# Kernel tuning notes

Hardware: AMD Instinct MI355X
Metric: run time of the kernel (lower is better)

The kernel has to match this reference:

```python
import jax, jax.numpy as jnp
import numpy as np

B, N, D_IN, D_MEM, LAYERS = 8, 2048, 128, 128, 3


def setup_inputs() -> dict:
    key = jax.random.key(0)
    k1, k2, k3, k4 = jax.random.split(key, 4)
    inputs = jax.random.normal(k1, (B, N, D_IN), dtype=jnp.float32)
    # attention-derived adjacency: nonnegative weights
    out_adj = jax.random.uniform(k2, (B, N, N), dtype=jnp.float32)
    # per-layer Linear weights (all layers 128->128 here, stacked) with
    # torch nn.Linear-style init scale 1/sqrt(fan_in)
    scale = 1.0 / np.sqrt(D_IN)
    W = jax.random.uniform(k3, (LAYERS, D_IN, D_MEM), minval=-scale, maxval=scale, dtype=jnp.float32)
    b = jax.random.uniform(k4, (LAYERS, D_MEM), minval=-scale, maxval=scale, dtype=jnp.float32)
    return {"inputs": inputs, "out_adj": out_adj, "W": W, "b": b}


def reference(inputs, out_adj, W, b):
    # GCN.forward (eval mode; dropout = identity)
    adj = out_adj  # [B, N, N]
    denom = jnp.sum(adj, axis=2, keepdims=True) + 1.0  # [B, N, 1]
    outputs = inputs  # [B, N, D]
    for l in range(W.shape[0]):
        Ax = jnp.einsum('bij,bjd->bid', adj, outputs)      # aggregate
        AxW = Ax @ W[l] + b[l]                             # per-layer linear
        outputs = jax.nn.relu(AxW / denom)                 # normalize + activate
    return outputs
```

## Files before the change

### kernel.cpp

```cpp
#include <hip/hip_runtime.h>

#define NN 2048
#define DD 128

typedef _Float16 f16x8 __attribute__((ext_vector_type(8)));
typedef float f32x4 __attribute__((ext_vector_type(4)));


__global__ __launch_bounds__(256) void prep_kernel(
    const float* __restrict__ W, _Float16* __restrict__ Wt) {
  int idx = blockIdx.x * 256 + threadIdx.x;
  int l = idx >> 14, r = idx & 16383, d = r >> 7, k = r & 127;
  Wt[idx] = (_Float16)W[l * 16384 + k * 128 + d];
}

__global__ __launch_bounds__(256) void prepAdj_kernel(
    const float* __restrict__ adj, _Float16* __restrict__ adjH,
    float* __restrict__ rdg) {
  __shared__ float rs[16][4];
  const int bx = blockIdx.x, tid = threadIdx.x;
  const int it = bx & 127, batch = bx >> 7;
  const int lane = tid & 63, wave = tid >> 6;
  const int quad = lane >> 4, l15 = lane & 15;

  const float* Ap = adj + ((size_t)(batch * NN) + it * 16 + l15) * NN + quad * 8;
  _Float16* Hp = adjH + (size_t)batch * NN * NN + ((size_t)it * 64) * 512 + lane * 8;

  float s = 0.f;
#pragma unroll
  for (int j = 0; j < 16; ++j) {
    const int ct = wave + 4 * j;
    float4 a0 = *(const float4*)(Ap + ct * 32);
    float4 a1 = *(const float4*)(Ap + ct * 32 + 4);
    s += ((a0.x + a0.y) + (a0.z + a0.w)) + ((a1.x + a1.y) + (a1.z + a1.w));
    f16x8 h = {(_Float16)a0.x, (_Float16)a0.y, (_Float16)a0.z, (_Float16)a0.w,
               (_Float16)a1.x, (_Float16)a1.y, (_Float16)a1.z, (_Float16)a1.w};
    *(f16x8*)(Hp + (size_t)ct * 512) = h;
  }
  s += __shfl_xor(s, 16);
  s += __shfl_xor(s, 32);
  if (lane < 16) rs[lane][wave] = s;
  __syncthreads();
  if (tid < 16) {
    float t = rs[tid][0] + rs[tid][1] + rs[tid][2] + rs[tid][3];
    rdg[batch * NN + it * 16 + tid] = 1.0f / (t + 1.0f);
  }
}

__global__ __launch_bounds__(256) void transposeX_kernel(
    const float* __restrict__ X, _Float16* __restrict__ Xt) {
  const int bx = blockIdx.x, tid = threadIdx.x;
  const int batch = bx & 7, nt = bx >> 3;
  const int lane = tid & 63, wave = tid >> 6;
  const int quad = lane >> 4, l15 = lane & 15;
  const size_t batA = (size_t)batch * (128 * NN);
#pragma unroll
  for (int dtl = 0; dtl < 2; ++dtl) {
    const int dt = wave * 2 + dtl;
    const float* Xp = X + ((size_t)(batch * NN) + nt * 32 + quad * 8) * DD + dt * 16 + l15;
    f16x8 v;
#pragma unroll
    for (int e = 0; e < 8; ++e) v[e] = (_Float16)Xp[(size_t)e * DD];
    *(f16x8*)(Xt + batA + ((size_t)(dt * 64 + nt)) * 512 + lane * 8) = v;
  }
}

__device__ __forceinline__ void epiGemm(const float (*Xs)[132],
    const _Float16* __restrict__ Wf, int d0, int quad, int l15,
    f32x4 (&o)[2][2]) {
#pragma unroll
  for (int kk = 0; kk < 128; kk += 32) {
    f16x8 a0 = *(const f16x8*)(Wf + (d0 + l15) * DD + kk + quad * 8);
    f16x8 a1 = *(const f16x8*)(Wf + (d0 + 16 + l15) * DD + kk + quad * 8);
#pragma unroll
    for (int fi = 0; fi < 2; ++fi) {
      const float* xp = &Xs[fi * 16 + l15][kk + quad * 8];
      f16x8 b = {(_Float16)xp[0], (_Float16)xp[1], (_Float16)xp[2], (_Float16)xp[3],
                 (_Float16)xp[4], (_Float16)xp[5], (_Float16)xp[6], (_Float16)xp[7]};
      o[0][fi] = __builtin_amdgcn_mfma_f32_16x16x32_f16(a0, b, o[0][fi], 0, 0, 0);
      o[1][fi] = __builtin_amdgcn_mfma_f32_16x16x32_f16(a1, b, o[1][fi], 0, 0, 0);
    }
  }
}

template<int MODE>
__global__ __launch_bounds__(256, 4) void aggT_kernel(
    const _Float16* __restrict__ adjH, const float* __restrict__ rdg,
    const _Float16* __restrict__ At, const float* __restrict__ bias,
    const _Float16* __restrict__ WA, const _Float16* __restrict__ WB,
    _Float16* __restrict__ Yout, float* __restrict__ out) {
  __shared__ float Xs[32][132];
  __shared__ float bsh[128];
  __shared__ float rdsh[32];

  const int tid = threadIdx.x, bx = blockIdx.x;
  const int batch = bx & 7, i0 = (bx >> 3) * 32;
  const int lane = tid & 63, wave = tid >> 6;
  const int quad = lane >> 4, l15 = lane & 15, d0 = wave * 32;

  const size_t batA = (size_t)batch * (128 * NN);
  const size_t batB = (size_t)batch * ((size_t)NN * NN);
  const int it0 = i0 >> 4;
  const _Float16* Ap0 = At + batA + ((size_t)(2 * wave) * 64) * 512 + lane * 8;
  const _Float16* Ap1 = At + batA + ((size_t)(2 * wave + 1) * 64) * 512 + lane * 8;
  const _Float16* Bp0 = adjH + batB + ((size_t)it0 * 64) * 512 + lane * 8;
  const _Float16* Bp1 = adjH + batB + ((size_t)(it0 + 1) * 64) * 512 + lane * 8;

  if (tid < 128) bsh[tid] = bias[tid];
  if (tid < 32) rdsh[tid] = rdg[batch * NN + i0 + tid];
  __syncthreads();

  f32x4 acc[2][2] = {};
  f16x8 qa0[2], qa1[2], qb0[2], qb1[2];
#define LDT(ct, s)                                  \
  { qa0[s] = *(const f16x8*)(Ap0 + (ct) * 512);     \
    qa1[s] = *(const f16x8*)(Ap1 + (ct) * 512);     \
    qb0[s] = *(const f16x8*)(Bp0 + (ct) * 512);     \
    qb1[s] = *(const f16x8*)(Bp1 + (ct) * 512); }
#define MMT(s)                                                                          \
  { acc[0][0] = __builtin_amdgcn_mfma_f32_16x16x32_f16(qa0[s], qb0[s], acc[0][0], 0, 0, 0); \
    acc[0][1] = __builtin_amdgcn_mfma_f32_16x16x32_f16(qa0[s], qb1[s], acc[0][1], 0, 0, 0); \
    acc[1][0] = __builtin_amdgcn_mfma_f32_16x16x32_f16(qa1[s], qb0[s], acc[1][0], 0, 0, 0); \
    acc[1][1] = __builtin_amdgcn_mfma_f32_16x16x32_f16(qa1[s], qb1[s], acc[1][1], 0, 0, 0); }

  LDT(0, 0)
  LDT(1, 1)
#pragma unroll
  for (int ct = 0; ct < 64; ct += 2) {
    MMT(0)
    if (ct + 2 < 64) LDT(ct + 2, 0)
    MMT(1)
    if (ct + 3 < 64) LDT(ct + 3, 1)
  }
#undef LDT
#undef MMT

  const float rv0 = rdsh[l15], rv1 = rdsh[16 + l15];

  f32x4 accY[2][2];

  if (MODE == 0) {
#pragma unroll
    for (int df = 0; df < 2; ++df)
#pragma unroll
      for (int fi = 0; fi < 2; ++fi)
#pragma unroll
        for (int r = 0; r < 4; ++r)
          Xs[fi * 16 + l15][d0 + df * 16 + quad * 4 + r] = acc[df][fi][r];
    __syncthreads();
    f32x4 acc2[2][2] = {};
    epiGemm(Xs, WA, d0, quad, l15, acc2);
    __syncthreads();
#pragma unroll
    for (int df = 0; df < 2; ++df)
#pragma unroll
      for (int fi = 0; fi < 2; ++fi)
#pragma unroll
        for (int r = 0; r < 4; ++r) {
          int d = d0 + df * 16 + quad * 4 + r;
          float rv = fi ? rv1 : rv0;
          Xs[fi * 16 + l15][d] = fmaxf((acc2[df][fi][r] + bsh[d]) * rv, 0.f);
        }
    __syncthreads();
    f32x4 acc3[2][2] = {};
    epiGemm(Xs, WB, d0, quad, l15, acc3);
#pragma unroll
    for (int df = 0; df < 2; ++df)
#pragma unroll
      for (int fi = 0; fi < 2; ++fi) accY[df][fi] = acc3[df][fi];
  } else {
#pragma unroll
    for (int df = 0; df < 2; ++df)
#pragma unroll
      for (int fi = 0; fi < 2; ++fi)
#pragma unroll
        for (int r = 0; r < 4; ++r) {
          int d = d0 + df * 16 + quad * 4 + r;
          float rv = fi ? rv1 : rv0;
          Xs[fi * 16 + l15][d] = fmaxf((acc[df][fi][r] + bsh[d]) * rv, 0.f);
        }
    __syncthreads();
    if (MODE == 2) {
      float* outB = out + (size_t)(batch * NN + i0) * DD;
#pragma unroll
      for (int u = 0; u < 4; ++u) {
        int c = tid + 256 * u;
        int i = c >> 5, f4 = (c & 31) * 4;
        *(float4*)(outB + (size_t)i * DD + f4) = *(const float4*)&Xs[i][f4];
      }
      return;
    }
    f32x4 acc2[2][2] = {};
    epiGemm(Xs, WA, d0, quad, l15, acc2);
#pragma unroll
    for (int df = 0; df < 2; ++df)
#pragma unroll
      for (int fi = 0; fi < 2; ++fi) accY[df][fi] = acc2[df][fi];
  }

  __syncthreads();
  _Float16* Yst = (_Float16*)Xs;
#pragma unroll
  for (int df = 0; df < 2; ++df)
#pragma unroll
    for (int fi = 0; fi < 2; ++fi)
#pragma unroll
      for (int r = 0; r < 4; ++r)
        Yst[(d0 + df * 16 + quad * 4 + r) * 40 + fi * 16 + l15] =
            (_Float16)accY[df][fi][r];
  __syncthreads();
  const int nt = i0 >> 5;
  _Float16* Yb = Yout + batA;
#pragma unroll
  for (int dtl = 0; dtl < 2; ++dtl) {
    const int dt = 2 * wave + dtl;
    f16x8 v = *(const f16x8*)(&Yst[(dt * 16 + l15) * 40 + quad * 8]);
    *(f16x8*)(Yb + ((size_t)(dt * 64 + nt)) * 512 + lane * 8) = v;
  }
}

__global__ __launch_bounds__(256) void gemmY_kernel(
    const float* __restrict__ X, const _Float16* __restrict__ Wt,
    _Float16* __restrict__ Yt) {
  const int bx = blockIdx.x;
  const int batch = bx & 7, n0 = (bx >> 3) * 32;
  const int tid = threadIdx.x, lane = tid & 63, wave = tid >> 6;
  const int quad = lane >> 4, l15 = lane & 15, d0 = wave * 32;
  const float* Xb = X + (size_t)(batch * NN + n0) * DD;
  f32x4 acc[2][2] = {};
#pragma unroll
  for (int kk = 0; kk < 128; kk += 32) {
    f16x8 a0 = *(const f16x8*)(Wt + (d0 + l15) * DD + kk + quad * 8);
    f16x8 a1 = *(const f16x8*)(Wt + (d0 + 16 + l15) * DD + kk + quad * 8);
#pragma unroll
    for (int fi = 0; fi < 2; ++fi) {
      const float* xp = Xb + (size_t)(fi * 16 + l15) * DD + kk + quad * 8;
      float4 x0 = *(const float4*)xp;
      float4 x1 = *(const float4*)(xp + 4);
      f16x8 b = {(_Float16)x0.x, (_Float16)x0.y, (_Float16)x0.z, (_Float16)x0.w,
                 (_Float16)x1.x, (_Float16)x1.y, (_Float16)x1.z, (_Float16)x1.w};
      acc[0][fi] = __builtin_amdgcn_mfma_f32_16x16x32_f16(a0, b, acc[0][fi], 0, 0, 0);
      acc[1][fi] = __builtin_amdgcn_mfma_f32_16x16x32_f16(a1, b, acc[1][fi], 0, 0, 0);
    }
  }
  _Float16* YtB = Yt + (size_t)batch * DD * NN;
#pragma unroll
  for (int df = 0; df < 2; ++df)
#pragma unroll
    for (int fi = 0; fi < 2; ++fi)
#pragma unroll
      for (int r = 0; r < 4; ++r)
        YtB[(size_t)(d0 + df * 16 + quad * 4 + r) * NN + n0 + fi * 16 + l15] =
            (_Float16)acc[df][fi][r];
}

template<bool LAST>
__global__ __launch_bounds__(256) void agg_kernel(
    const float* __restrict__ adj, const _Float16* __restrict__ Yt,
    const float* __restrict__ bias, const _Float16* __restrict__ Wn,
    _Float16* __restrict__ Ytn, float* __restrict__ out) {
  __shared__ _Float16 Bs[2][32 * 64];
  __shared__ float Xs[32][132];
  __shared__ float bsh[128];
  __shared__ float rd[32];

  const int tid = threadIdx.x, bx = blockIdx.x;
  const int batch = bx & 7, i0 = (bx >> 3) * 32;
  const int lane = tid & 63, wave = tid >> 6;
  const int quad = lane >> 4, l15 = lane & 15, d0 = wave * 32;
  const int ai = tid >> 3, ac = tid & 7;
  const int sc = ac ^ (ai & 7);

  const float* adjR = adj + (size_t)(batch * NN + i0 + ai) * NN + ac * 8;
  const _Float16* YtB = Yt + (size_t)batch * DD * NN;
  const _Float16* Ya0 = YtB + (size_t)(d0 + l15) * NN;
  const _Float16* Ya1 = YtB + (size_t)(d0 + 16 + l15) * NN;

  if (tid < 128) bsh[tid] = bias[tid];

  f32x4 acc[2][2] = {};
  float rowsum = 0.f;

  float4 av0 = *(const float4*)(adjR);
  float4 av1 = *(const float4*)(adjR + 4);
  f16x8 a[2][2];
#pragma unroll
  for (int k2 = 0; k2 < 2; ++k2) {
    a[k2][0] = *(const f16x8*)(Ya0 + k2 * 32 + quad * 8);
    a[k2][1] = *(const f16x8*)(Ya1 + k2 * 32 + quad * 8);
  }

  for (int ko = 0; ko < 32; ++ko) {
    rowsum += ((av0.x + av0.y) + (av0.z + av0.w)) + ((av1.x + av1.y) + (av1.z + av1.w));
    f16x8 h = {(_Float16)av0.x, (_Float16)av0.y, (_Float16)av0.z, (_Float16)av0.w,
               (_Float16)av1.x, (_Float16)av1.y, (_Float16)av1.z, (_Float16)av1.w};
    *(f16x8*)(&Bs[ko & 1][ai * 64 + sc * 8]) = h;
    f16x8 an[2][2];
    if (ko < 31) {
      const int kb = (ko + 1) * 64;
      av0 = *(const float4*)(adjR + kb);
      av1 = *(const float4*)(adjR + kb + 4);
#pragma unroll
      for (int k2 = 0; k2 < 2; ++k2) {
        an[k2][0] = *(const f16x8*)(Ya0 + kb + k2 * 32 + quad * 8);
        an[k2][1] = *(const f16x8*)(Ya1 + kb + k2 * 32 + quad * 8);
      }
    }
    __syncthreads();
    const _Float16* B = Bs[ko & 1];
#pragma unroll
    for (int k2 = 0; k2 < 2; ++k2)
#pragma unroll
      for (int fi = 0; fi < 2; ++fi) {
        const int row = fi * 16 + l15;
        const int ch = (k2 * 4 + quad) ^ (row & 7);
        f16x8 b = *(const f16x8*)(&B[row * 64 + ch * 8]);
        acc[0][fi] = __builtin_amdgcn_mfma_f32_16x16x32_f16(a[k2][0], b, acc[0][fi], 0, 0, 0);
        acc[1][fi] = __builtin_amdgcn_mfma_f32_16x16x32_f16(a[k2][1], b, acc[1][fi], 0, 0, 0);
      }
#pragma unroll
    for (int k2 = 0; k2 < 2; ++k2) { a[k2][0] = an[k2][0]; a[k2][1] = an[k2][1]; }
  }

  rowsum += __shfl_xor(rowsum, 1);
  rowsum += __shfl_xor(rowsum, 2);
  rowsum += __shfl_xor(rowsum, 4);
  if (ac == 0) rd[ai] = 1.0f / (rowsum + 1.0f);
  __syncthreads();

#pragma unroll
  for (int df = 0; df < 2; ++df)
#pragma unroll
    for (int fi = 0; fi < 2; ++fi)
#pragma unroll
      for (int r = 0; r < 4; ++r) {
        int d = d0 + df * 16 + quad * 4 + r;
        int i = fi * 16 + l15;
        Xs[i][d] = fmaxf((acc[df][fi][r] + bsh[d]) * rd[i], 0.f);
      }
  __syncthreads();

  if (LAST) {
    float* outB = out + (size_t)(batch * NN + i0) * DD;
#pragma unroll
    for (int u = 0; u < 4; ++u) {
      int c = tid + 256 * u;
      int i = c >> 5, f4 = (c & 31) * 4;
      *(float4*)(outB + (size_t)i * DD + f4) = *(const float4*)&Xs[i][f4];
    }
  } else {
    f32x4 acc2[2][2] = {};
    epiGemm(Xs, Wn, d0, quad, l15, acc2);
    _Float16* YnB = Ytn + (size_t)batch * DD * NN;
#pragma unroll
    for (int df = 0; df < 2; ++df)
#pragma unroll
      for (int fi = 0; fi < 2; ++fi)
#pragma unroll
        for (int r = 0; r < 4; ++r)
          YnB[(size_t)(d0 + df * 16 + quad * 4 + r) * NN + i0 + fi * 16 + l15] =
              (_Float16)acc2[df][fi][r];
  }
}

extern "C" void kernel_launch(void* const* d_in, const int* in_sizes, int n_in,
                              void* d_out, int out_size, void* d_ws, size_t ws_size,
                              hipStream_t stream) {
  const float* x0   = (const float*)d_in[0];
  const float* adj  = (const float*)d_in[1];
  const float* W    = (const float*)d_in[2];
  const float* bias = (const float*)d_in[3];
  float* out = (float*)d_out;

  _Float16* Wt   = (_Float16*)d_ws;
  float*    rdg  = (float*)((char*)d_ws + (1u << 17));
  _Float16* Xt   = (_Float16*)((char*)d_ws + (1u << 20));
  _Float16* Y1t  = (_Float16*)((char*)d_ws + (5u << 20));
  _Float16* Y2t  = (_Float16*)((char*)d_ws + (9u << 20));
  _Float16* adjH = (_Float16*)((char*)d_ws + (16u << 20));

  const bool big = ws_size >= (80ull << 20);

  dim3 blk(256);
  prep_kernel<<<192, blk, 0, stream>>>(W, Wt);
  if (big) {
    prepAdj_kernel  <<<1024, blk, 0, stream>>>(adj, adjH, rdg);
    transposeX_kernel<<<512, blk, 0, stream>>>(x0, Xt);
    aggT_kernel<0><<<512, blk, 0, stream>>>(adjH, rdg, Xt, bias, Wt, Wt + 16384, Y1t, nullptr);
    aggT_kernel<1><<<512, blk, 0, stream>>>(adjH, rdg, Y1t, bias + 128, Wt + 32768, nullptr, Y2t, nullptr);
    aggT_kernel<2><<<512, blk, 0, stream>>>(adjH, rdg, Y2t, bias + 256, nullptr, nullptr, nullptr, out);
  } else {
    _Float16* YtA  = Xt;
    _Float16* YtB_ = (_Float16*)d_out;
    gemmY_kernel<<<512, blk, 0, stream>>>(x0, Wt, YtA);
    agg_kernel<false><<<512, blk, 0, stream>>>(adj, YtA,  bias,       Wt + 16384, YtB_, nullptr);
    agg_kernel<false><<<512, blk, 0, stream>>>(adj, YtB_, bias + 128, Wt + 32768, YtA,  nullptr);
    agg_kernel<true ><<<512, blk, 0, stream>>>(adj, YtA,  bias + 256, nullptr,    nullptr, out);
  }
}
```

Before: 294.4 us.

## Stage adjacency tiles through LDS in aggregation and merge prep kernels

The aggregation kernel now has two waves load each adjacency fp16 tile once into a double-buffered LDS slot, and all four waves read it from there. Before, every wave loaded both adjacency fragments directly from global memory. The adjacency and X transpose prep kernels are also merged into one launch to save a kernel launch. In exchange there is a __syncthreads every k-step, the loop is no longer unrolled with deep register prefetch, and the occupancy hint is dropped, which may expose latency. The workspace threshold also moves up by 1 MiB.

```diff
diff --git a/kernel.cpp b/kernel.cpp
--- a/kernel.cpp
+++ b/kernel.cpp
@@ -14,54 +14,51 @@
   Wt[idx] = (_Float16)W[l * 16384 + k * 128 + d];
 }
 
-__global__ __launch_bounds__(256) void prepAdj_kernel(
+__global__ __launch_bounds__(256) void prepAll_kernel(
     const float* __restrict__ adj, _Float16* __restrict__ adjH,
-    float* __restrict__ rdg) {
+    float* __restrict__ rdg, const float* __restrict__ X,
+    _Float16* __restrict__ Xt) {
   __shared__ float rs[16][4];
   const int bx = blockIdx.x, tid = threadIdx.x;
-  const int it = bx & 127, batch = bx >> 7;
   const int lane = tid & 63, wave = tid >> 6;
   const int quad = lane >> 4, l15 = lane & 15;
 
-  const float* Ap = adj + ((size_t)(batch * NN) + it * 16 + l15) * NN + quad * 8;
-  _Float16* Hp = adjH + (size_t)batch * NN * NN + ((size_t)it * 64) * 512 + lane * 8;
-
-  float s = 0.f;
-#pragma unroll
-  for (int j = 0; j < 16; ++j) {
-    const int ct = wave + 4 * j;
-    float4 a0 = *(const float4*)(Ap + ct * 32);
-    float4 a1 = *(const float4*)(Ap + ct * 32 + 4);
-    s += ((a0.x + a0.y) + (a0.z + a0.w)) + ((a1.x + a1.y) + (a1.z + a1.w));
-    f16x8 h = {(_Float16)a0.x, (_Float16)a0.y, (_Float16)a0.z, (_Float16)a0.w,
-               (_Float16)a1.x, (_Float16)a1.y, (_Float16)a1.z, (_Float16)a1.w};
-    *(f16x8*)(Hp + (size_t)ct * 512) = h;
-  }
-  s += __shfl_xor(s, 16);
-  s += __shfl_xor(s, 32);
-  if (lane < 16) rs[lane][wave] = s;
-  __syncthreads();
-  if (tid < 16) {
-    float t = rs[tid][0] + rs[tid][1] + rs[tid][2] + rs[tid][3];
-    rdg[batch * NN + it * 16 + tid] = 1.0f / (t + 1.0f);
-  }
-}
-
-__global__ __launch_bounds__(256) void transposeX_kernel(
-    const float* __restrict__ X, _Float16* __restrict__ Xt) {
-  const int bx = blockIdx.x, tid = threadIdx.x;
-  const int batch = bx & 7, nt = bx >> 3;
-  const int lane = tid & 63, wave = tid >> 6;
-  const int quad = lane >> 4, l15 = lane & 15;
-  const size_t batA = (size_t)batch * (128 * NN);
-#pragma unroll
-  for (int dtl = 0; dtl < 2; ++dtl) {
-    const int dt = wave * 2 + dtl;
-    const float* Xp = X + ((size_t)(batch * NN) + nt * 32 + quad * 8) * DD + dt * 16 + l15;
-    f16x8 v;
-#pragma unroll
-    for (int e = 0; e < 8; ++e) v[e] = (_Float16)Xp[(size_t)e * DD];
-    *(f16x8*)(Xt + batA + ((size_t)(dt * 64 + nt)) * 512 + lane * 8) = v;
+  if (bx < 1024) {
+    const int it = bx & 127, batch = bx >> 7;
+    const float* Ap = adj + ((size_t)(batch * NN) + it * 16 + l15) * NN + quad * 8;
+    _Float16* Hp = adjH + (size_t)batch * NN * NN + ((size_t)it * 64) * 512 + lane * 8;
+    float s = 0.f;
+#pragma unroll
+    for (int j = 0; j < 16; ++j) {
+      const int ct = wave + 4 * j;
+      float4 a0 = *(const float4*)(Ap + ct * 32);
+      float4 a1 = *(const float4*)(Ap + ct * 32 + 4);
+      s += ((a0.x + a0.y) + (a0.z + a0.w)) + ((a1.x + a1.y) + (a1.z + a1.w));
+      f16x8 h = {(_Float16)a0.x, (_Float16)a0.y, (_Float16)a0.z, (_Float16)a0.w,
+                 (_Float16)a1.x, (_Float16)a1.y, (_Float16)a1.z, (_Float16)a1.w};
+      *(f16x8*)(Hp + (size_t)ct * 512) = h;
+    }
+    s += __shfl_xor(s, 16);
+    s += __shfl_xor(s, 32);
+    if (lane < 16) rs[lane][wave] = s;
+    __syncthreads();
+    if (tid < 16) {
+      float t = rs[tid][0] + rs[tid][1] + rs[tid][2] + rs[tid][3];
+      rdg[batch * NN + it * 16 + tid] = 1.0f / (t + 1.0f);
+    }
+  } else if (bx < 1536) {
+    const int vbx = bx - 1024;
+    const int batch = vbx & 7, nt = vbx >> 3;
+    const size_t batA = (size_t)batch * (128 * NN);
+#pragma unroll
+    for (int dtl = 0; dtl < 2; ++dtl) {
+      const int dt = wave * 2 + dtl;
+      const float* Xp = X + ((size_t)(batch * NN) + nt * 32 + quad * 8) * DD + dt * 16 + l15;
+      f16x8 v;
+#pragma unroll
+      for (int e = 0; e < 8; ++e) v[e] = (_Float16)Xp[(size_t)e * DD];
+      *(f16x8*)(Xt + batA + ((size_t)(dt * 64 + nt)) * 512 + lane * 8) = v;
+    }
   }
 }
 
@@ -84,59 +81,66 @@
 }
 
 template<int MODE>
-__global__ __launch_bounds__(256, 4) void aggT_kernel(
+__global__ __launch_bounds__(256) void aggL_kernel(
     const _Float16* __restrict__ adjH, const float* __restrict__ rdg,
     const _Float16* __restrict__ At, const float* __restrict__ bias,
     const _Float16* __restrict__ WA, const _Float16* __restrict__ WB,
     _Float16* __restrict__ Yout, float* __restrict__ out) {
+  __shared__ _Float16 Bs[2][1024];
   __shared__ float Xs[32][132];
   __shared__ float bsh[128];
   __shared__ float rdsh[32];
 
   const int tid = threadIdx.x, bx = blockIdx.x;
-  const int batch = bx & 7, i0 = (bx >> 3) * 32;
+  const int batch = bx & 7, iblk = bx >> 3, i0 = iblk * 32;
   const int lane = tid & 63, wave = tid >> 6;
   const int quad = lane >> 4, l15 = lane & 15, d0 = wave * 32;
 
   const size_t batA = (size_t)batch * (128 * NN);
   const size_t batB = (size_t)batch * ((size_t)NN * NN);
-  const int it0 = i0 >> 4;
   const _Float16* Ap0 = At + batA + ((size_t)(2 * wave) * 64) * 512 + lane * 8;
   const _Float16* Ap1 = At + batA + ((size_t)(2 * wave + 1) * 64) * 512 + lane * 8;
-  const _Float16* Bp0 = adjH + batB + ((size_t)it0 * 64) * 512 + lane * 8;
-  const _Float16* Bp1 = adjH + batB + ((size_t)(it0 + 1) * 64) * 512 + lane * 8;
+  const _Float16* BpW = adjH + batB + ((size_t)(iblk * 2 + wave) * 64) * 512 + lane * 8;
 
   if (tid < 128) bsh[tid] = bias[tid];
   if (tid < 32) rdsh[tid] = rdg[batch * NN + i0 + tid];
+
+  if (wave < 2) {
+    f16x8 h0 = *(const f16x8*)(BpW);
+    *(f16x8*)&Bs[0][wave * 512 + lane * 8] = h0;
+  }
+  f16x8 aC0 = *(const f16x8*)(Ap0);
+  f16x8 aC1 = *(const f16x8*)(Ap1);
+  f32x4 acc[2][2] = {};
   __syncthreads();
 
-  f32x4 acc[2][2] = {};
-  f16x8 qa0[2], qa1[2], qb0[2], qb1[2];
-#define LDT(ct, s)                                  \
-  { qa0[s] = *(const f16x8*)(Ap0 + (ct) * 512);     \
-    qa1[s] = *(const f16x8*)(Ap1 + (ct) * 512);     \
-    qb0[s] = *(const f16x8*)(Bp0 + (ct) * 512);     \
-    qb1[s] = *(const f16x8*)(Bp1 + (ct) * 512); }
-#define MMT(s)                                                                          \
-  { acc[0][0] = __builtin_amdgcn_mfma_f32_16x16x32_f16(qa0[s], qb0[s], acc[0][0], 0, 0, 0); \
-    acc[0][1] = __builtin_amdgcn_mfma_f32_16x16x32_f16(qa0[s], qb1[s], acc[0][1], 0, 0, 0); \
-    acc[1][0] = __builtin_amdgcn_mfma_f32_16x16x32_f16(qa1[s], qb0[s], acc[1][0], 0, 0, 0); \
-    acc[1][1] = __builtin_amdgcn_mfma_f32_16x16x32_f16(qa1[s], qb1[s], acc[1][1], 0, 0, 0); }
-
-  LDT(0, 0)
-  LDT(1, 1)
-#pragma unroll
+#define STEP(ct, CB, NB)                                                                   \
+  {                                                                                        \
+    const bool stg = (wave < 2) && ((ct) < 63);                                            \
+    f16x8 hN = {};                                                                         \
+    if (stg) hN = *(const f16x8*)(BpW + ((ct) + 1) * 512);                                 \
+    const int ctn = ((ct) < 63) ? (ct) + 1 : (ct);                                         \
+    f16x8 aN0 = *(const f16x8*)(Ap0 + ctn * 512);                                          \
+    f16x8 aN1 = *(const f16x8*)(Ap1 + ctn * 512);                                          \
+    f16x8 b0 = *(const f16x8*)&Bs[CB][lane * 8];                                           \
+    f16x8 b1 = *(const f16x8*)&Bs[CB][512 + lane * 8];                                     \
+    acc[0][0] = __builtin_amdgcn_mfma_f32_16x16x32_f16(aC0, b0, acc[0][0], 0, 0, 0);       \
+    acc[0][1] = __builtin_amdgcn_mfma_f32_16x16x32_f16(aC0, b1, acc[0][1], 0, 0, 0);       \
+    acc[1][0] = __builtin_amdgcn_mfma_f32_16x16x32_f16(aC1, b0, acc[1][0], 0, 0, 0);       \
+    acc[1][1] = __builtin_amdgcn_mfma_f32_16x16x32_f16(aC1, b1, acc[1][1], 0, 0, 0);       \
+    if (stg) *(f16x8*)&Bs[NB][wave * 512 + lane * 8] = hN;                                 \
+    __syncthreads();                                                                       \
+    aC0 = aN0;                                                                             \
+    aC1 = aN1;                                                                             \
+  }
+
   for (int ct = 0; ct < 64; ct += 2) {
-    MMT(0)
-    if (ct + 2 < 64) LDT(ct + 2, 0)
-    MMT(1)
-    if (ct + 3 < 64) LDT(ct + 3, 1)
-  }
-#undef LDT
-#undef MMT
+    STEP(ct, 0, 1)
+    STEP(ct + 1, 1, 0)
+  }
+#undef STEP
 
   const float rv0 = rdsh[l15], rv1 = rdsh[16 + l15];
-
   f32x4 accY[2][2];
 
   if (MODE == 0) {
@@ -259,7 +263,7 @@
     const float* __restrict__ adj, const _Float16* __restrict__ Yt,
     const float* __restrict__ bias, const _Float16* __restrict__ Wn,
     _Float16* __restrict__ Ytn, float* __restrict__ out) {
-  __shared__ _Float16 Bs[2][32 * 64];
+  __shared__ _Float16 Bsl[2][32 * 64];
   __shared__ float Xs[32][132];
   __shared__ float bsh[128];
   __shared__ float rd[32];
@@ -294,7 +298,7 @@
     rowsum += ((av0.x + av0.y) + (av0.z + av0.w)) + ((av1.x + av1.y) + (av1.z + av1.w));
     f16x8 h = {(_Float16)av0.x, (_Float16)av0.y, (_Float16)av0.z, (_Float16)av0.w,
                (_Float16)av1.x, (_Float16)av1.y, (_Float16)av1.z, (_Float16)av1.w};
-    *(f16x8*)(&Bs[ko & 1][ai * 64 + sc * 8]) = h;
+    *(f16x8*)(&Bsl[ko & 1][ai * 64 + sc * 8]) = h;
     f16x8 an[2][2];
     if (ko < 31) {
       const int kb = (ko + 1) * 64;
@@ -307,7 +311,7 @@
       }
     }
     __syncthreads();
-    const _Float16* B = Bs[ko & 1];
+    const _Float16* B = Bsl[ko & 1];
 #pragma unroll
     for (int k2 = 0; k2 < 2; ++k2)
 #pragma unroll
@@ -379,16 +383,15 @@
   _Float16* Y2t  = (_Float16*)((char*)d_ws + (9u << 20));
   _Float16* adjH = (_Float16*)((char*)d_ws + (16u << 20));
 
-  const bool big = ws_size >= (80ull << 20);
+  const bool big = ws_size >= (81ull << 20);
 
   dim3 blk(256);
   prep_kernel<<<192, blk, 0, stream>>>(W, Wt);
   if (big) {
-    prepAdj_kernel  <<<1024, blk, 0, stream>>>(adj, adjH, rdg);
-    transposeX_kernel<<<512, blk, 0, stream>>>(x0, Xt);
-    aggT_kernel<0><<<512, blk, 0, stream>>>(adjH, rdg, Xt, bias, Wt, Wt + 16384, Y1t, nullptr);
-    aggT_kernel<1><<<512, blk, 0, stream>>>(adjH, rdg, Y1t, bias + 128, Wt + 32768, nullptr, Y2t, nullptr);
-    aggT_kernel<2><<<512, blk, 0, stream>>>(adjH, rdg, Y2t, bias + 256, nullptr, nullptr, nullptr, out);
+    prepAll_kernel<<<1536, blk, 0, stream>>>(adj, adjH, rdg, x0, Xt);
+    aggL_kernel<0><<<512, blk, 0, stream>>>(adjH, rdg, Xt, bias, Wt, Wt + 16384, Y1t, nullptr);
+    aggL_kernel<1><<<512, blk, 0, stream>>>(adjH, rdg, Y1t, bias + 128, Wt + 32768, nullptr, Y2t, nullptr);
+    aggL_kernel<2><<<512, blk, 0, stream>>>(adjH, rdg, Y2t, bias + 256, nullptr, nullptr, nullptr, out);
   } else {
     _Float16* YtA  = Xt;
     _Float16* YtB_ = (_Float16*)d_out;
```

After: 294.4 us. No clear change (-0.0%).
